# Kernel optimization log

Measured on AMD Instinct MI355X. Metric: run time of the kernel, lower is better.

Reference implementation:

```python
import jax, jax.numpy as jnp
import numpy as np

WAVELET_LEN = 64
N_SCALES = 8
MIN_SCALE, MAX_SCALE = 1.0, 32.0
SPARSITY_THRESHOLD = 1e-4


def _morlet_bank():
    # matches AdaptiveWaveletTransform._initialize_mother_wavelets
    t = jnp.linspace(-4.0, 4.0, WAVELET_LEN)
    i = jnp.arange(N_SCALES, dtype=jnp.float32)
    omega = 2.0 + i * 0.5           # [n_scales]
    sigma = 1.0 + i * 0.1
    w = jnp.exp(-t[None, :] ** 2 / (2.0 * sigma[:, None] ** 2)) * jnp.cos(omega[:, None] * t[None, :])
    return w / jnp.linalg.norm(w, axis=1, keepdims=True)  # [n_scales, 64]


def setup_inputs() -> dict:
    key = jax.random.key(0)
    signal = jax.random.normal(key, (16, 4096, 64), dtype=jnp.float32)
    mother_wavelets = _morlet_bank().astype(jnp.float32)   # learned param
    scale_weights = jnp.ones((N_SCALES,), dtype=jnp.float32)  # learned param
    return {"signal": signal, "mother_wavelets": mother_wavelets, "scale_weights": scale_weights}


def reference(signal, mother_wavelets, scale_weights):
    # scales are static (registered buffer) -> compute in numpy
    scales = np.logspace(np.log10(MIN_SCALE), np.log10(MAX_SCALE), N_SCALES)
    B, S, F = signal.shape
    per_scale = []
    grid = jnp.arange(WAVELET_LEN, dtype=jnp.float32)
    for idx in range(N_SCALES):
        scale = float(scales[idx])
        L = int(WAVELET_LEN * scale)  # dilated kernel length (static)
        # F.interpolate(mode='linear', align_corners=True): sample at linspace(0, 63, L)
        xq = jnp.linspace(0.0, WAVELET_LEN - 1.0, L)
        kern = jnp.interp(xq, grid, mother_wavelets[idx]) / np.sqrt(scale)  # [L]
        n = S + L - 1                      # full conv length
        n_fft = 1 << int(np.ceil(np.log2(n)))  # next pow2 (static)
        # vectorized FFT conv over batch and features simultaneously
        sig_f = jnp.fft.rfft(signal, n=n_fft, axis=1)      # [B, n_fft//2+1, F]
        k_f = jnp.fft.rfft(kern, n=n_fft)                   # [n_fft//2+1]
        conv = jnp.fft.irfft(sig_f * k_f[None, :, None], n=n_fft, axis=1)
        per_scale.append(conv[:, :S, :])   # L>=64 so n>=S always
    coeffs = jnp.stack(per_scale, axis=1)  # [B, n_scales, S, F]
    coeffs = coeffs * scale_weights[None, :, None, None]
    # use_sparse + eval-mode thresholding
    mask = (jnp.abs(coeffs) > SPARSITY_THRESHOLD).astype(coeffs.dtype)
    return coeffs * mask
```

## Files before the change

kernel.cpp:

```cpp
#include <hip/hip_runtime.h>
#include <hip/hip_bf16.h>
#include <math.h>

#define S_LEN 4096
#define N_FEAT 64
#define N_BATCH 16
#define N_SCALES 8
#define THRESH 1e-4f
#define PADL 2048
#define NCHUNK ((PADL + S_LEN) / 16)
#define BCHUNK_ELEMS 1024

typedef unsigned short ushort_t;
typedef __attribute__((ext_vector_type(8))) short bf16x8;
typedef __attribute__((ext_vector_type(16))) float f32x16;

struct ScaleParams {
    int L[N_SCALES], Mc[N_SCALES], Niter[N_SCALES], Aoff[N_SCALES];
    float inv_sqrt_scale[N_SCALES], step[N_SCALES];
};

__global__ void prep_A(const float* __restrict__ mother, ushort_t* __restrict__ Atab,
                       ScaleParams p, int totalA) {
    int i = blockIdx.x * blockDim.x + threadIdx.x;
    if (i >= totalA) return;
    int idx = 0;
#pragma unroll
    for (int s = 1; s < N_SCALES; ++s)
        if (i >= p.Aoff[s]) idx = s;
    int rel = i - p.Aoff[idx];
    int ci = rel >> 9;
    int r = rel & 511;
    int lane = r >> 3, e = r & 7;
    int ti = lane & 31, sj = 8 * (lane >> 5) + e;
    int kidx = 16 * (ci - 6) - 16 + ti - sj;
    float v = 0.f;
    if (kidx >= 0 && kidx < p.L[idx]) {
        float xq = fminf(kidx * p.step[idx], 63.0f);
        int i0 = (int)xq; if (i0 > 62) i0 = 62;
        float frac = xq - (float)i0;
        float a = mother[idx * 64 + i0];
        float b = mother[idx * 64 + i0 + 1];
        v = (a + (b - a) * frac) * p.inv_sqrt_scale[idx];
    }
    __hip_bfloat16 hh = __float2bfloat16(v);
    Atab[i] = *reinterpret_cast<ushort_t*>(&hh);
}

__global__ __launch_bounds__(256) void transpose_sig(const float* __restrict__ sig,
                                                     ushort_t* __restrict__ XTc) {
    const int b = blockIdx.y;
    const int G = blockIdx.x * 4 + (threadIdx.x >> 6);
    const int l = threadIdx.x & 63;
    unsigned int u[4];
    if (G < PADL / 8) {
        u[0] = u[1] = u[2] = u[3] = 0u;
    } else {
        const float* sp = sig + ((size_t)b * S_LEN + ((size_t)G * 8 - PADL)) * N_FEAT + l;
#pragma unroll
        for (int j = 0; j < 4; ++j) {
            float v0 = sp[(size_t)(2 * j) * N_FEAT];
            float v1 = sp[(size_t)(2 * j + 1) * N_FEAT];
            __hip_bfloat16 h0 = __float2bfloat16(v0);
            __hip_bfloat16 h1 = __float2bfloat16(v1);
            u[j] = (unsigned int)*reinterpret_cast<ushort_t*>(&h0) |
                   ((unsigned int)*reinterpret_cast<ushort_t*>(&h1) << 16);
        }
    }
    uint4 vv = {u[0], u[1], u[2], u[3]};
    *reinterpret_cast<uint4*>(XTc + (size_t)b * (NCHUNK * BCHUNK_ELEMS)
                              + (size_t)G * 512 + l * 8) = vv;
}

#define MFMA(A, X, C) C = __builtin_amdgcn_mfma_f32_32x32x16_bf16(A, X, C, 0, 0, 0)

__global__ __launch_bounds__(256) void wavelet_mfma(
    const ushort_t* __restrict__ XTc, const ushort_t* __restrict__ Atab,
    const float* __restrict__ sw, float* __restrict__ out, ScaleParams p) {
    const int idx = 7 - blockIdx.z;
    const int b = blockIdx.y;
    const int wave = threadIdx.x >> 6, lane = threadIdx.x & 63;
    const int tw0 = blockIdx.x * 512 + wave * 128;
    const int h = lane >> 5, fc = lane & 31;
    const int niter = p.Niter[idx];
    const int c0 = (PADL + tw0) / 16 + 1;

    const ushort_t* Ab = Atab + p.Aoff[idx] + lane * 8;
    const ushort_t* Bb = XTc + (size_t)b * (NCHUNK * BCHUNK_ELEMS)
                       + h * 512 + fc * 8;

    f32x16 c00, c01, c10, c11, c20, c21, c30, c31;
#pragma unroll
    for (int r = 0; r < 16; ++r) {
        c00[r] = 0.f; c01[r] = 0.f; c10[r] = 0.f; c11[r] = 0.f;
        c20[r] = 0.f; c21[r] = 0.f; c30[r] = 0.f; c31[r] = 0.f;
    }

    bf16x8 Ar[8];
#pragma unroll
    for (int i = 0; i < 8; ++i)
        Ar[i] = *reinterpret_cast<const bf16x8*>(Ab + i * 512);
    bf16x8 Xe0 = *reinterpret_cast<const bf16x8*>(Bb + (size_t)(c0 + 6) * 1024);
    bf16x8 Xe1 = *reinterpret_cast<const bf16x8*>(Bb + (size_t)(c0 + 6) * 1024 + 256);
    bf16x8 Xo0 = *reinterpret_cast<const bf16x8*>(Bb + (size_t)(c0 + 5) * 1024);
    bf16x8 Xo1 = *reinterpret_cast<const bf16x8*>(Bb + (size_t)(c0 + 5) * 1024 + 256);

    const ushort_t* Apf = Ab + 8 * 512;
    const ushort_t* Bpf = Bb + (size_t)(c0 + 4) * 1024;

    for (int it = 0; it < niter; it += 8) {
#pragma unroll
        for (int ph = 0; ph < 8; ++ph) {
            bf16x8 a0 = Ar[ph & 7];
            bf16x8 a1 = Ar[(ph + 2) & 7];
            bf16x8 a2 = Ar[(ph + 4) & 7];
            bf16x8 a3 = Ar[(ph + 6) & 7];
            bf16x8 x0 = (ph & 1) ? Xo0 : Xe0;
            bf16x8 x1 = (ph & 1) ? Xo1 : Xe1;
            Ar[ph & 7] = *reinterpret_cast<const bf16x8*>(Apf);
            Apf += 512;
            if (ph & 1) {
                Xo0 = *reinterpret_cast<const bf16x8*>(Bpf);
                Xo1 = *reinterpret_cast<const bf16x8*>(Bpf + 256);
            } else {
                Xe0 = *reinterpret_cast<const bf16x8*>(Bpf);
                Xe1 = *reinterpret_cast<const bf16x8*>(Bpf + 256);
            }
            Bpf -= 1024;
            MFMA(a0, x0, c00); MFMA(a0, x1, c01);
            MFMA(a1, x0, c10); MFMA(a1, x1, c11);
            MFMA(a2, x0, c20); MFMA(a2, x1, c21);
            MFMA(a3, x0, c30); MFMA(a3, x1, c31);
        }
    }

    const float w = sw[idx];
    float* ob = out + ((size_t)(b * N_SCALES + idx) * S_LEN + tw0) * N_FEAT + fc;
#define STORE_TILE(CLO, CHI, JT)                                               \
    {                                                                          \
        _Pragma("unroll") for (int r = 0; r < 16; ++r) {                       \
            const int row = (JT) * 32 + (r & 3) + 8 * (r >> 2) + 4 * h;        \
            float v;                                                           \
            v = CLO[r] * w; v = (fabsf(v) > THRESH) ? v : 0.f;                 \
            __builtin_nontemporal_store(v, &ob[(size_t)row * N_FEAT]);         \
            v = CHI[r] * w; v = (fabsf(v) > THRESH) ? v : 0.f;                 \
            __builtin_nontemporal_store(v, &ob[(size_t)row * N_FEAT + 32]);    \
        }                                                                      \
    }
    STORE_TILE(c00, c01, 0)
    STORE_TILE(c10, c11, 1)
    STORE_TILE(c20, c21, 2)
    STORE_TILE(c30, c31, 3)
#undef STORE_TILE
}

extern "C" void kernel_launch(void* const* d_in, const int* in_sizes, int n_in,
                              void* d_out, int out_size, void* d_ws, size_t ws_size,
                              hipStream_t stream) {
    const float* sig    = (const float*)d_in[0];
    const float* mother = (const float*)d_in[1];
    const float* sw     = (const float*)d_in[2];
    float* out = (float*)d_out;

    ushort_t* Atab = (ushort_t*)((char*)d_ws + 32768);
    ushort_t* XTc  = (ushort_t*)((char*)d_ws + 524288);

    ScaleParams p;
    int aoff = 0;
    for (int i = 0; i < N_SCALES; ++i) {
        double scale = pow(10.0, (double)i * log10(32.0) / 7.0);
        double v = 64.0 * scale;
        double r = floor(v + 0.5);
        int L = (fabs(v - r) < 1e-6) ? (int)r : (int)v;
        p.L[i] = L;
        p.Mc[i] = (L + 46) >> 4;
        p.Niter[i] = (p.Mc[i] + 13) & ~7;
        p.Aoff[i] = aoff;
        aoff += (p.Niter[i] + 8) * 512;
        p.inv_sqrt_scale[i] = (float)(1.0 / sqrt(scale));
        p.step[i] = (float)(63.0 / (double)(L - 1));
    }
    const int totalA = aoff;

    prep_A<<<dim3((totalA + 255) / 256), dim3(256), 0, stream>>>(
        mother, Atab, p, totalA);
    transpose_sig<<<dim3((PADL + S_LEN) / 32, N_BATCH), dim3(256), 0, stream>>>(
        sig, XTc);

    wavelet_mfma<<<dim3(S_LEN / 512, N_BATCH, N_SCALES), dim3(256), 0, stream>>>(
        XTc, Atab, sw, out, p);
}
```

Baseline: 87.93 us.

## Remap blocks to XCDs by batch and deepen signal prefetch to four stages

The 3D grid becomes a 1D grid, and the block index is decoded so that each XCD (block index mod 8) handles two batches. Blocks that share a batch's signal data then land on the same XCD's L2, which should improve cache reuse. The signal register prefetch also grows from a double buffer to a four-deep ring, hiding more global-load latency at the cost of extra VGPRs. Scheduling order within each XCD still runs the largest scales first.

After: 71.44 us. 18.7% less time.

```diff
diff --git a/kernel.cpp b/kernel.cpp
--- a/kernel.cpp
+++ b/kernel.cpp
@@ -77,10 +77,16 @@
 __global__ __launch_bounds__(256) void wavelet_mfma(
     const ushort_t* __restrict__ XTc, const ushort_t* __restrict__ Atab,
     const float* __restrict__ sw, float* __restrict__ out, ScaleParams p) {
-    const int idx = 7 - blockIdx.z;
-    const int b = blockIdx.y;
+    const int n = blockIdx.x;
+    const int xcd = n & 7;
+    const int r = n >> 3;
+    const int b = 2 * xcd + (r & 1);
+    const int q = r >> 1;
+    const int xblk = q & 7;
+    const int idx = 7 - (q >> 3);
+
     const int wave = threadIdx.x >> 6, lane = threadIdx.x & 63;
-    const int tw0 = blockIdx.x * 512 + wave * 128;
+    const int tw0 = xblk * 512 + wave * 128;
     const int h = lane >> 5, fc = lane & 31;
     const int niter = p.Niter[idx];
     const int c0 = (PADL + tw0) / 16 + 1;
@@ -91,22 +97,25 @@
 
     f32x16 c00, c01, c10, c11, c20, c21, c30, c31;
 #pragma unroll
-    for (int r = 0; r < 16; ++r) {
-        c00[r] = 0.f; c01[r] = 0.f; c10[r] = 0.f; c11[r] = 0.f;
-        c20[r] = 0.f; c21[r] = 0.f; c30[r] = 0.f; c31[r] = 0.f;
+    for (int i = 0; i < 16; ++i) {
+        c00[i] = 0.f; c01[i] = 0.f; c10[i] = 0.f; c11[i] = 0.f;
+        c20[i] = 0.f; c21[i] = 0.f; c30[i] = 0.f; c31[i] = 0.f;
     }
 
     bf16x8 Ar[8];
 #pragma unroll
     for (int i = 0; i < 8; ++i)
         Ar[i] = *reinterpret_cast<const bf16x8*>(Ab + i * 512);
-    bf16x8 Xe0 = *reinterpret_cast<const bf16x8*>(Bb + (size_t)(c0 + 6) * 1024);
-    bf16x8 Xe1 = *reinterpret_cast<const bf16x8*>(Bb + (size_t)(c0 + 6) * 1024 + 256);
-    bf16x8 Xo0 = *reinterpret_cast<const bf16x8*>(Bb + (size_t)(c0 + 5) * 1024);
-    bf16x8 Xo1 = *reinterpret_cast<const bf16x8*>(Bb + (size_t)(c0 + 5) * 1024 + 256);
+    bf16x8 Xr0[4], Xr1[4];
+#pragma unroll
+    for (int i = 0; i < 4; ++i) {
+        const ushort_t* q0 = Bb + (size_t)(c0 + 6 - i) * 1024;
+        Xr0[i] = *reinterpret_cast<const bf16x8*>(q0);
+        Xr1[i] = *reinterpret_cast<const bf16x8*>(q0 + 256);
+    }
 
     const ushort_t* Apf = Ab + 8 * 512;
-    const ushort_t* Bpf = Bb + (size_t)(c0 + 4) * 1024;
+    const ushort_t* Bpf = Bb + (size_t)(c0 + 2) * 1024;
 
     for (int it = 0; it < niter; it += 8) {
 #pragma unroll
@@ -115,17 +124,12 @@
             bf16x8 a1 = Ar[(ph + 2) & 7];
             bf16x8 a2 = Ar[(ph + 4) & 7];
             bf16x8 a3 = Ar[(ph + 6) & 7];
-            bf16x8 x0 = (ph & 1) ? Xo0 : Xe0;
-            bf16x8 x1 = (ph & 1) ? Xo1 : Xe1;
+            bf16x8 x0 = Xr0[ph & 3];
+            bf16x8 x1 = Xr1[ph & 3];
             Ar[ph & 7] = *reinterpret_cast<const bf16x8*>(Apf);
             Apf += 512;
-            if (ph & 1) {
-                Xo0 = *reinterpret_cast<const bf16x8*>(Bpf);
-                Xo1 = *reinterpret_cast<const bf16x8*>(Bpf + 256);
-            } else {
-                Xe0 = *reinterpret_cast<const bf16x8*>(Bpf);
-                Xe1 = *reinterpret_cast<const bf16x8*>(Bpf + 256);
-            }
+            Xr0[ph & 3] = *reinterpret_cast<const bf16x8*>(Bpf);
+            Xr1[ph & 3] = *reinterpret_cast<const bf16x8*>(Bpf + 256);
             Bpf -= 1024;
             MFMA(a0, x0, c00); MFMA(a0, x1, c01);
             MFMA(a1, x0, c10); MFMA(a1, x1, c11);
@@ -138,12 +142,12 @@
     float* ob = out + ((size_t)(b * N_SCALES + idx) * S_LEN + tw0) * N_FEAT + fc;
 #define STORE_TILE(CLO, CHI, JT)                                               \
     {                                                                          \
-        _Pragma("unroll") for (int r = 0; r < 16; ++r) {                       \
-            const int row = (JT) * 32 + (r & 3) + 8 * (r >> 2) + 4 * h;        \
+        _Pragma("unroll") for (int i = 0; i < 16; ++i) {                       \
+            const int row = (JT) * 32 + (i & 3) + 8 * (i >> 2) + 4 * h;        \
             float v;                                                           \
-            v = CLO[r] * w; v = (fabsf(v) > THRESH) ? v : 0.f;                 \
+            v = CLO[i] * w; v = (fabsf(v) > THRESH) ? v : 0.f;                 \
             __builtin_nontemporal_store(v, &ob[(size_t)row * N_FEAT]);         \
-            v = CHI[r] * w; v = (fabsf(v) > THRESH) ? v : 0.f;                 \
+            v = CHI[i] * w; v = (fabsf(v) > THRESH) ? v : 0.f;                 \
             __builtin_nontemporal_store(v, &ob[(size_t)row * N_FEAT + 32]);    \
         }                                                                      \
     }
@@ -187,6 +191,6 @@
     transpose_sig<<<dim3((PADL + S_LEN) / 32, N_BATCH), dim3(256), 0, stream>>>(
         sig, XTc);
 
-    wavelet_mfma<<<dim3(S_LEN / 512, N_BATCH, N_SCALES), dim3(256), 0, stream>>>(
+    wavelet_mfma<<<dim3(S_LEN / 512 * N_BATCH * N_SCALES), dim3(256), 0, stream>>>(
         XTc, Atab, sw, out, p);
 }
```

## Halve per-wave time tile, swap MFMA operands for vector stores, XCD-aware grid

Applied to the files above, without the earlier changes.

Each wave now computes 64 time rows instead of 128, so the accumulator and A-register footprint halve and twice as many blocks launch. The launch bounds request 4 blocks per CU to raise occupancy. The grid becomes 1D with a mapping that keeps two batches' blocks on the same XCD, so the signal data each XCD reads stays in its L2. MFMA operands are swapped so the accumulator layout lets results be written as 16-byte vector nontemporal stores. The A table offset and Niter padding are shrunk to match the smaller prefetch depth, at the cost of re-reading the A table more often per output row.

Result: slower. 179.9 us (+104.6%).

```diff
diff --git a/kernel.cpp b/kernel.cpp
--- a/kernel.cpp
+++ b/kernel.cpp
@@ -14,6 +14,7 @@
 typedef unsigned short ushort_t;
 typedef __attribute__((ext_vector_type(8))) short bf16x8;
 typedef __attribute__((ext_vector_type(16))) float f32x16;
+typedef __attribute__((ext_vector_type(4))) float f32x4;
 
 struct ScaleParams {
     int L[N_SCALES], Mc[N_SCALES], Niter[N_SCALES], Aoff[N_SCALES];
@@ -33,7 +34,7 @@
     int r = rel & 511;
     int lane = r >> 3, e = r & 7;
     int ti = lane & 31, sj = 8 * (lane >> 5) + e;
-    int kidx = 16 * (ci - 6) - 16 + ti - sj;
+    int kidx = 16 * (ci - 2) - 16 + ti - sj;
     float v = 0.f;
     if (kidx >= 0 && kidx < p.L[idx]) {
         float xq = fminf(kidx * p.step[idx], 63.0f);
@@ -74,13 +75,19 @@
 
 #define MFMA(A, X, C) C = __builtin_amdgcn_mfma_f32_32x32x16_bf16(A, X, C, 0, 0, 0)
 
-__global__ __launch_bounds__(256) void wavelet_mfma(
+__global__ __launch_bounds__(256, 4) void wavelet_mfma(
     const ushort_t* __restrict__ XTc, const ushort_t* __restrict__ Atab,
     const float* __restrict__ sw, float* __restrict__ out, ScaleParams p) {
-    const int idx = 7 - blockIdx.z;
-    const int b = blockIdx.y;
+    const int n = blockIdx.x;
+    const int xcd = n & 7;
+    const int r = n >> 3;
+    const int b = 2 * xcd + (r & 1);
+    const int q = r >> 1;
+    const int xblk = q & 15;
+    const int idx = 7 - (q >> 4);
+
     const int wave = threadIdx.x >> 6, lane = threadIdx.x & 63;
-    const int tw0 = blockIdx.x * 512 + wave * 128;
+    const int tw0 = xblk * 256 + wave * 64;
     const int h = lane >> 5, fc = lane & 31;
     const int niter = p.Niter[idx];
     const int c0 = (PADL + tw0) / 16 + 1;
@@ -89,35 +96,30 @@
     const ushort_t* Bb = XTc + (size_t)b * (NCHUNK * BCHUNK_ELEMS)
                        + h * 512 + fc * 8;
 
-    f32x16 c00, c01, c10, c11, c20, c21, c30, c31;
+    f32x16 c00, c01, c10, c11;
 #pragma unroll
-    for (int r = 0; r < 16; ++r) {
-        c00[r] = 0.f; c01[r] = 0.f; c10[r] = 0.f; c11[r] = 0.f;
-        c20[r] = 0.f; c21[r] = 0.f; c30[r] = 0.f; c31[r] = 0.f;
-    }
+    for (int i = 0; i < 16; ++i) { c00[i] = 0.f; c01[i] = 0.f; c10[i] = 0.f; c11[i] = 0.f; }
 
-    bf16x8 Ar[8];
+    bf16x8 Ar[4];
 #pragma unroll
-    for (int i = 0; i < 8; ++i)
+    for (int i = 0; i < 4; ++i)
         Ar[i] = *reinterpret_cast<const bf16x8*>(Ab + i * 512);
-    bf16x8 Xe0 = *reinterpret_cast<const bf16x8*>(Bb + (size_t)(c0 + 6) * 1024);
-    bf16x8 Xe1 = *reinterpret_cast<const bf16x8*>(Bb + (size_t)(c0 + 6) * 1024 + 256);
-    bf16x8 Xo0 = *reinterpret_cast<const bf16x8*>(Bb + (size_t)(c0 + 5) * 1024);
-    bf16x8 Xo1 = *reinterpret_cast<const bf16x8*>(Bb + (size_t)(c0 + 5) * 1024 + 256);
+    bf16x8 Xe0 = *reinterpret_cast<const bf16x8*>(Bb + (size_t)(c0 + 2) * 1024);
+    bf16x8 Xe1 = *reinterpret_cast<const bf16x8*>(Bb + (size_t)(c0 + 2) * 1024 + 256);
+    bf16x8 Xo0 = *reinterpret_cast<const bf16x8*>(Bb + (size_t)(c0 + 1) * 1024);
+    bf16x8 Xo1 = *reinterpret_cast<const bf16x8*>(Bb + (size_t)(c0 + 1) * 1024 + 256);
 
-    const ushort_t* Apf = Ab + 8 * 512;
-    const ushort_t* Bpf = Bb + (size_t)(c0 + 4) * 1024;
+    const ushort_t* Apf = Ab + 4 * 512;
+    const ushort_t* Bpf = Bb + (size_t)c0 * 1024;
 
     for (int it = 0; it < niter; it += 8) {
 #pragma unroll
         for (int ph = 0; ph < 8; ++ph) {
-            bf16x8 a0 = Ar[ph & 7];
-            bf16x8 a1 = Ar[(ph + 2) & 7];
-            bf16x8 a2 = Ar[(ph + 4) & 7];
-            bf16x8 a3 = Ar[(ph + 6) & 7];
+            bf16x8 a0 = Ar[ph & 3];
+            bf16x8 a1 = Ar[(ph + 2) & 3];
             bf16x8 x0 = (ph & 1) ? Xo0 : Xe0;
             bf16x8 x1 = (ph & 1) ? Xo1 : Xe1;
-            Ar[ph & 7] = *reinterpret_cast<const bf16x8*>(Apf);
+            Ar[ph & 3] = *reinterpret_cast<const bf16x8*>(Apf);
             Apf += 512;
             if (ph & 1) {
                 Xo0 = *reinterpret_cast<const bf16x8*>(Bpf);
@@ -127,30 +129,32 @@
                 Xe1 = *reinterpret_cast<const bf16x8*>(Bpf + 256);
             }
             Bpf -= 1024;
-            MFMA(a0, x0, c00); MFMA(a0, x1, c01);
-            MFMA(a1, x0, c10); MFMA(a1, x1, c11);
-            MFMA(a2, x0, c20); MFMA(a2, x1, c21);
-            MFMA(a3, x0, c30); MFMA(a3, x1, c31);
+            MFMA(x0, a0, c00); MFMA(x1, a0, c01);
+            MFMA(x0, a1, c10); MFMA(x1, a1, c11);
         }
     }
 
     const float w = sw[idx];
-    float* ob = out + ((size_t)(b * N_SCALES + idx) * S_LEN + tw0) * N_FEAT + fc;
-#define STORE_TILE(CLO, CHI, JT)                                               \
-    {                                                                          \
-        _Pragma("unroll") for (int r = 0; r < 16; ++r) {                       \
-            const int row = (JT) * 32 + (r & 3) + 8 * (r >> 2) + 4 * h;        \
-            float v;                                                           \
-            v = CLO[r] * w; v = (fabsf(v) > THRESH) ? v : 0.f;                 \
-            __builtin_nontemporal_store(v, &ob[(size_t)row * N_FEAT]);         \
-            v = CHI[r] * w; v = (fabsf(v) > THRESH) ? v : 0.f;                 \
-            __builtin_nontemporal_store(v, &ob[(size_t)row * N_FEAT + 32]);    \
-        }                                                                      \
+    float* ob = out + ((size_t)(b * N_SCALES + idx) * S_LEN + tw0) * N_FEAT;
+#define STORE_TILE(ACC, J, F)                                                   \
+    {                                                                           \
+        const size_t trow = (size_t)((J) * 32 + fc) * N_FEAT + (F) * 32 + 4 * h;\
+        _Pragma("unroll") for (int qd = 0; qd < 4; ++qd) {                      \
+            f32x4 vv;                                                           \
+            float t0_ = ACC[4 * qd + 0] * w, t1_ = ACC[4 * qd + 1] * w;         \
+            float t2_ = ACC[4 * qd + 2] * w, t3_ = ACC[4 * qd + 3] * w;         \
+            vv.x = (fabsf(t0_) > THRESH) ? t0_ : 0.f;                           \
+            vv.y = (fabsf(t1_) > THRESH) ? t1_ : 0.f;                           \
+            vv.z = (fabsf(t2_) > THRESH) ? t2_ : 0.f;                           \
+            vv.w = (fabsf(t3_) > THRESH) ? t3_ : 0.f;                           \
+            __builtin_nontemporal_store(vv,                                     \
+                reinterpret_cast<f32x4*>(&ob[trow + 8 * qd]));                  \
+        }                                                                       \
     }
-    STORE_TILE(c00, c01, 0)
-    STORE_TILE(c10, c11, 1)
-    STORE_TILE(c20, c21, 2)
-    STORE_TILE(c30, c31, 3)
+    STORE_TILE(c00, 0, 0)
+    STORE_TILE(c01, 0, 1)
+    STORE_TILE(c10, 1, 0)
+    STORE_TILE(c11, 1, 1)
 #undef STORE_TILE
 }
 
@@ -174,7 +178,7 @@
         int L = (fabs(v - r) < 1e-6) ? (int)r : (int)v;
         p.L[i] = L;
         p.Mc[i] = (L + 46) >> 4;
-        p.Niter[i] = (p.Mc[i] + 13) & ~7;
+        p.Niter[i] = (p.Mc[i] + 9) & ~7;
         p.Aoff[i] = aoff;
         aoff += (p.Niter[i] + 8) * 512;
         p.inv_sqrt_scale[i] = (float)(1.0 / sqrt(scale));
@@ -187,6 +191,6 @@
     transpose_sig<<<dim3((PADL + S_LEN) / 32, N_BATCH), dim3(256), 0, stream>>>(
         sig, XTc);
 
-    wavelet_mfma<<<dim3(S_LEN / 512, N_BATCH, N_SCALES), dim3(256), 0, stream>>>(
+    wavelet_mfma<<<dim3(S_LEN / 256 * N_BATCH * N_SCALES), dim3(256), 0, stream>>>(
         XTc, Atab, sw, out, p);
 }
```
